# Optimization experiments

Hardware: AMD Instinct MI355X
Metric: run time of the kernel (lower is better)

Reference implementation:

```python
import jax, jax.numpy as jnp
import numpy as np

N_NODES = 100000
N_EDGES = 3200000
N_GRAPHS = 256
FEAT = 128
HIDDEN = 128
N_CLASSES = 10


def setup_inputs() -> dict:
    key = jax.random.key(0)
    ks = jax.random.split(key, 12)
    x = jax.random.normal(ks[0], (N_NODES, FEAT), dtype=jnp.float32)
    edge_index = jax.random.randint(ks[1], (2, N_EDGES), 0, N_NODES, dtype=jnp.int64)
    batch = jnp.sort(jax.random.randint(ks[2], (N_NODES,), 0, N_GRAPHS, dtype=jnp.int64))
    s = 0.05
    return {
        "x": x,
        "edge_index": edge_index,
        "batch": batch,
        "W1": jax.random.normal(ks[3], (FEAT, HIDDEN), dtype=jnp.float32) * s,
        "b1": jnp.zeros((HIDDEN,), dtype=jnp.float32),
        "W2": jax.random.normal(ks[4], (HIDDEN, HIDDEN), dtype=jnp.float32) * s,
        "b2": jnp.zeros((HIDDEN,), dtype=jnp.float32),
        "W3": jax.random.normal(ks[5], (HIDDEN, HIDDEN), dtype=jnp.float32) * s,
        "b3": jnp.zeros((HIDDEN,), dtype=jnp.float32),
        "lin1_w": jax.random.normal(ks[6], (HIDDEN, HIDDEN), dtype=jnp.float32) * s,
        "lin1_b": jnp.zeros((HIDDEN,), dtype=jnp.float32),
        "lin2_w": jax.random.normal(ks[7], (HIDDEN, N_CLASSES), dtype=jnp.float32) * s,
        "lin2_b": jnp.zeros((N_CLASSES,), dtype=jnp.float32),
    }


def _gcn_norm(edge_index, n_nodes):
    # PyG GCNConv default: add self-loops, symmetric normalization.
    src = jnp.concatenate([edge_index[0], jnp.arange(n_nodes, dtype=edge_index.dtype)])
    dst = jnp.concatenate([edge_index[1], jnp.arange(n_nodes, dtype=edge_index.dtype)])
    deg = jax.ops.segment_sum(jnp.ones_like(dst, dtype=jnp.float32), dst, num_segments=n_nodes)
    dis = jnp.where(deg > 0, jax.lax.rsqrt(jnp.maximum(deg, 1.0)), 0.0)
    norm = dis[src] * dis[dst]  # [E + N]
    return src, dst, norm


def _gcn_conv(x, src, dst, norm, W, b, n_nodes):
    h = x @ W                               # [N, H]
    msg = h[src] * norm[:, None]            # gather + scale, [E+N, H]
    out = jax.ops.segment_sum(msg, dst, num_segments=n_nodes)  # scatter-add
    return out + b


def reference(x, edge_index, batch, W1, b1, W2, b2, W3, b3, lin1_w, lin1_b, lin2_w, lin2_b):
    n = x.shape[0]
    src, dst, norm = _gcn_norm(edge_index, n)
    h = jax.nn.relu(_gcn_conv(x, src, dst, norm, W1, b1, n))
    h = jax.nn.relu(_gcn_conv(h, src, dst, norm, W2, b2, n))
    h = jax.nn.relu(_gcn_conv(h, src, dst, norm, W3, b3, n))
    # global mean pool over graphs
    sums = jax.ops.segment_sum(h, batch, num_segments=N_GRAPHS)
    cnts = jax.ops.segment_sum(jnp.ones((n,), dtype=h.dtype), batch, num_segments=N_GRAPHS)
    g = sums / jnp.maximum(cnts, 1.0)[:, None]
    g = jax.nn.relu(g @ lin1_w + lin1_b)
    # dropout p=0.5 is identity at inference
    return g @ lin2_w + lin2_b
```

## Files before the change

### kernel.cpp

```cpp
#include <hip/hip_runtime.h>
#include <hip/hip_fp16.h>

#define FEAT 128
#define CHUNK 8192
#define BSH 7
#define CAP 6144
#define RSTRIDE 784

#define QS  16.0f
#define QSI 0.0625f

typedef _Float16 half8 __attribute__((ext_vector_type(8)));
typedef float floatx4 __attribute__((ext_vector_type(4)));
typedef float floatx2 __attribute__((ext_vector_type(2)));

__device__ __forceinline__ unsigned int enc8x4(float a, float b, float c, float d) {
  unsigned int r = __builtin_amdgcn_cvt_pk_fp8_f32(a, b, 0u, false);
  return __builtin_amdgcn_cvt_pk_fp8_f32(c, d, r, true);
}
__device__ __forceinline__ void acc8(unsigned int w, float* a) {
  floatx2 v0 = __builtin_amdgcn_cvt_pk_f32_fp8(w, false);
  floatx2 v1 = __builtin_amdgcn_cvt_pk_f32_fp8(w, true);
  a[0] += v0.x; a[1] += v0.y; a[2] += v1.x; a[3] += v1.y;
}


__global__ __launch_bounds__(256) void sort_prep_kernel(
    const int* __restrict__ ei, int E, int nchunks, int nbuk,
    int* __restrict__ pairs, int* __restrict__ runs,
    const float* __restrict__ W1, const float* __restrict__ W2,
    const float* __restrict__ W3, _Float16* __restrict__ P1,
    _Float16* __restrict__ P2, _Float16* __restrict__ P3,
    unsigned char* __restrict__ qA, unsigned char* __restrict__ qB, int N) {
  __shared__ int lhist[1024];
  __shared__ int lofs[1024];
  __shared__ int lcur[1024];
  __shared__ int tsum[256];
  __shared__ int stage[CHUNK];
  int t = threadIdx.x;
  if ((int)blockIdx.x >= nchunks) {
    int b = blockIdx.x - nchunks;
    if (b == 24) {
      if (t < 16) ((unsigned long long*)(qA + (size_t)N * FEAT))[t] = 0ull;
      else if (t < 32) ((unsigned long long*)(qB + (size_t)N * FEAT))[t - 16] = 0ull;
      return;
    }
    const float* W = (b < 8) ? W1 : (b < 16) ? W2 : W3;
    _Float16* P = (b < 8) ? P1 : (b < 16) ? P2 : P3;
    int e = (b & 7) * 256 + t;
    int l = e & 63;
    int ks = (e >> 6) & 3;
    int tn = e >> 8;
    int n = tn * 16 + (l & 15);
    int k0 = ks * 32 + (l >> 4) * 8;
    half8 v;
#pragma unroll
    for (int j = 0; j < 8; ++j) v[j] = (_Float16)W[(k0 + j) * 128 + n];
    *(half8*)(P + (size_t)e * 8) = v;
    return;
  }
  int c = blockIdx.x;
  int e0 = c * CHUNK;
  int e1 = e0 + CHUNK; if (e1 > E) e1 = E;
  int cnt = e1 - e0;
#pragma unroll
  for (int u = 0; u < 4; ++u) lhist[t + u * 256] = 0;
  __syncthreads();
  for (int j = e0 + t; j < e1; j += 256) atomicAdd(&lhist[ei[E + j] >> BSH], 1);
  __syncthreads();
  int a0 = lhist[4 * t], a1 = lhist[4 * t + 1];
  int a2 = lhist[4 * t + 2], a3 = lhist[4 * t + 3];
  int s = ((a0 + a1) + (a2 + a3));
  tsum[t] = s;
  __syncthreads();
  for (int o = 1; o < 256; o <<= 1) {
    int x = (t >= o) ? tsum[t - o] : 0;
    __syncthreads();
    tsum[t] += x;
    __syncthreads();
  }
  int base = tsum[t] - s;
  lofs[4 * t] = base;       lcur[4 * t] = base;
  lofs[4 * t + 1] = base + a0;           lcur[4 * t + 1] = base + a0;
  lofs[4 * t + 2] = base + a0 + a1;      lcur[4 * t + 2] = base + a0 + a1;
  lofs[4 * t + 3] = base + a0 + a1 + a2; lcur[4 * t + 3] = base + a0 + a1 + a2;
  __syncthreads();
  for (int k = t; k < nbuk; k += 256) runs[(size_t)c * RSTRIDE + k] = lofs[k];
  if (t == 0) runs[(size_t)c * RSTRIDE + nbuk] = cnt;
  for (int j = e0 + t; j < e1; j += 256) {
    int sv = ei[j];
    int d = ei[E + j];
    int p = atomicAdd(&lcur[d >> BSH], 1);
    stage[p] = sv | ((d & 127) << 24);
  }
  __syncthreads();
  for (int j = t; j < cnt; j += 256) pairs[e0 + j] = stage[j];
}

__global__ __launch_bounds__(256) void bucket_csr_kernel(
    const int* __restrict__ pairs, const int* __restrict__ runs, int nchunks,
    int nbuk, int2* __restrict__ row_se, float* __restrict__ dis,
    int* __restrict__ col, int N) {
  __shared__ int rs[512], rl[512], ro[512];
  __shared__ int cnt2[2048];
  __shared__ int tsum[256];
  __shared__ int stage[CAP];
  int b = blockIdx.x, t = threadIdx.x;
  for (int c = t; c < 512; c += 256) {
    int s0 = 0, len = 0;
    if (c < nchunks) {
      const int* rr = runs + (size_t)c * RSTRIDE;
      s0 = rr[b];
      len = rr[b + 1] - s0;
    }
    rs[c] = s0; rl[c] = len;
  }
#pragma unroll
  for (int u = 0; u < 8; ++u) cnt2[t + u * 256] = 0;
  __syncthreads();
  ro[t] = rl[t]; ro[t + 256] = rl[t + 256];
  __syncthreads();
  for (int o = 1; o < 512; o <<= 1) {
    int v0 = (t >= o) ? ro[t - o] : 0;
    int v1 = (t + 256 >= o) ? ro[t + 256 - o] : 0;
    __syncthreads();
    ro[t] += v0; ro[t + 256] += v1;
    __syncthreads();
  }
  int ce = ro[511];
  int y0 = ro[t] - rl[t];
  int y1 = ro[t + 256] - rl[t + 256];
  __syncthreads();
  ro[t] = y0; ro[t + 256] = y1;
  __syncthreads();
  int colbase = b * CAP;
  bool fits = ce <= CAP;
  if (fits) {
    for (int c = t; c < nchunks; c += 256) {
      int gs = c * CHUNK + rs[c];
      int base = ro[c];
      int len = rl[c];
      for (int j = 0; j < len; ++j) {
        int p = pairs[gs + j];
        stage[base + j] = p;
        int key = (((unsigned)p) >> 24) * 16 + ((p & 0xFFFFFF) >> 13);
        atomicAdd(&cnt2[key], 1);
      }
    }
  } else {
    for (int c = t; c < nchunks; c += 256) {
      int gs = c * CHUNK + rs[c];
      for (int j = 0; j < rl[c]; ++j) {
        int p = pairs[gs + j];
        int key = (((unsigned)p) >> 24) * 16 + ((p & 0xFFFFFF) >> 13);
        atomicAdd(&cnt2[key], 1);
      }
    }
  }
  __syncthreads();
  int av[8];
#pragma unroll
  for (int u = 0; u < 8; ++u) av[u] = cnt2[t * 8 + u];
  int s = 0;
#pragma unroll
  for (int u = 0; u < 8; ++u) s += av[u];
  tsum[t] = s;
  __syncthreads();
  for (int o = 1; o < 256; o <<= 1) {
    int x = (t >= o) ? tsum[t - o] : 0;
    __syncthreads();
    tsum[t] += x;
    __syncthreads();
  }
  int run = tsum[t] - s;
#pragma unroll
  for (int u = 0; u < 8; ++u) { int tmp = av[u]; cnt2[t * 8 + u] = run; run += tmp; }
  __syncthreads();
  if (t < 128) {
    int startv = cnt2[t * 16];
    int endv = (t == 127) ? ce : cnt2[t * 16 + 16];
    int node = b * 128 + t;
    if (node < N) {
      row_se[node] = make_int2(colbase + startv, colbase + endv);
      dis[node] = rsqrtf((float)(endv - startv + 1));
    }
  }
  __syncthreads();
  if (fits) {
    for (int j = t; j < ce; j += 256) {
      int p = stage[j];
      int src = p & 0xFFFFFF;
      int key = (((unsigned)p) >> 24) * 16 + (src >> 13);
      int loc = atomicAdd(&cnt2[key], 1);
      col[colbase + loc] = src << 7;
    }
  } else {
    for (int c = t; c < nchunks; c += 256) {
      int gs = c * CHUNK + rs[c];
      for (int j = 0; j < rl[c]; ++j) {
        int p = pairs[gs + j];
        int src = p & 0xFFFFFF;
        int key = (((unsigned)p) >> 24) * 16 + (src >> 13);
        int loc = atomicAdd(&cnt2[key], 1);
        if (loc < CAP) col[colbase + loc] = src << 7;
      }
    }
  }
}


__global__ __launch_bounds__(256) void mm1_kernel(
    const float* __restrict__ Av, const _Float16* __restrict__ Wpk,
    const float* __restrict__ scale, unsigned char* __restrict__ C, int N) {
  int t = threadIdx.x;
  int wave = t >> 6, lane = t & 63;
  int quad = lane >> 4, nidx = lane & 15;
  int m0 = blockIdx.x * 64 + wave * 16;
  int arow = m0 + nidx;
  bool avalid = arow < N;
  floatx4 acc[8];
#pragma unroll
  for (int tn = 0; tn < 8; ++tn) acc[tn] = (floatx4){0.f, 0.f, 0.f, 0.f};
#pragma unroll
  for (int ks = 0; ks < 4; ++ks) {
    half8 x = {};
    if (avalid) {
      const float* p = Av + (size_t)arow * 128 + ks * 32 + quad * 8;
      float4 f0 = *(const float4*)p;
      float4 f1 = *(const float4*)(p + 4);
      x[0] = (_Float16)f0.x; x[1] = (_Float16)f0.y;
      x[2] = (_Float16)f0.z; x[3] = (_Float16)f0.w;
      x[4] = (_Float16)f1.x; x[5] = (_Float16)f1.y;
      x[6] = (_Float16)f1.z; x[7] = (_Float16)f1.w;
    }
#pragma unroll
    for (int tn = 0; tn < 8; ++tn) {
      half8 wfrag = *(const half8*)(Wpk + ((size_t)((tn * 4 + ks) * 64 + lane)) * 8);
      acc[tn] = __builtin_amdgcn_mfma_f32_16x16x32_f16(wfrag, x, acc[tn], 0, 0, 0);
    }
  }
  if (avalid) {
    float s = scale[arow] * QS;
#pragma unroll
    for (int tn = 0; tn < 8; ++tn) {
      unsigned int r = enc8x4(acc[tn][0] * s, acc[tn][1] * s,
                              acc[tn][2] * s, acc[tn][3] * s);
      *(unsigned int*)(C + (size_t)arow * 128 + tn * 16 + quad * 4) = r;
    }
  }
}

__global__ __launch_bounds__(256) void agg_fuse_kernel(
    const unsigned char* __restrict__ hs_in, const int2* __restrict__ row_se,
    const int* __restrict__ col, const float* __restrict__ dis,
    const float* __restrict__ bias, const _Float16* __restrict__ Wpk,
    unsigned char* __restrict__ hs_out, int N) {
  __shared__ _Float16 Xs[32][136];
  int t = threadIdx.x;
  int wave = t >> 6, lane = t & 63;
  int lin = lane & 7;
  int nl = wave * 8 + (lane >> 3);
  int node = blockIdx.x * 32 + nl;
  bool valid = node < N;
  int lin16 = lin * 16;
  int zoff = N << 7;
  float a[16];
#pragma unroll
  for (int j = 0; j < 16; ++j) a[j] = 0.f;
  int selfoff = (valid ? (node << 7) : zoff) + lin16;
  uint4 s0 = *(const uint4*)(hs_in + (unsigned)selfoff);
  acc8(s0.x, a); acc8(s0.y, a + 4); acc8(s0.z, a + 8); acc8(s0.w, a + 12);
  int2 se = valid ? row_se[node] : make_int2(0, 0);
  int i = se.x, e = se.y;
  while (__any(i < e)) {
    int c[8];
#pragma unroll
    for (int u = 0; u < 8; ++u) {
      int idx = i + u;
      c[u] = (idx < e) ? col[idx] : zoff;
    }
    uint4 r[8];
#pragma unroll
    for (int u = 0; u < 8; ++u)
      r[u] = *(const uint4*)(hs_in + (unsigned)(c[u] + lin16));
#pragma unroll
    for (int u = 0; u < 8; ++u) {
      acc8(r[u].x, a);     acc8(r[u].y, a + 4);
      acc8(r[u].z, a + 8); acc8(r[u].w, a + 12);
    }
    i += 8;
  }
  float d = valid ? dis[node] * QSI : 0.f;
  const float* bp = bias + lin16;
  half8 hx0, hx1;
#pragma unroll
  for (int j = 0; j < 8; ++j) {
    float o0 = valid ? fmaxf(fmaf(d, a[j], bp[j]), 0.f) : 0.f;
    float o1 = valid ? fmaxf(fmaf(d, a[j + 8], bp[j + 8]), 0.f) : 0.f;
    hx0[j] = (_Float16)o0;
    hx1[j] = (_Float16)o1;
  }
  *(half8*)&Xs[nl][lin16] = hx0;
  *(half8*)&Xs[nl][lin16 + 8] = hx1;
  __syncthreads();
  int quad = lane >> 4, nidx = lane & 15;
  int ntile = wave >> 1;
  int f0 = (wave & 1) * 4;
  floatx4 acc[4];
#pragma unroll
  for (int f = 0; f < 4; ++f) acc[f] = (floatx4){0.f, 0.f, 0.f, 0.f};
#pragma unroll
  for (int ks = 0; ks < 4; ++ks) {
    half8 x = *(const half8*)&Xs[ntile * 16 + nidx][ks * 32 + quad * 8];
#pragma unroll
    for (int f = 0; f < 4; ++f) {
      half8 wf = *(const half8*)(Wpk + ((size_t)(((f0 + f) * 4 + ks) * 64 + lane)) * 8);
      acc[f] = __builtin_amdgcn_mfma_f32_16x16x32_f16(wf, x, acc[f], 0, 0, 0);
    }
  }
  int onode = blockIdx.x * 32 + ntile * 16 + nidx;
  if (onode < N) {
    float sc = dis[onode] * QS;
#pragma unroll
    for (int f = 0; f < 4; ++f) {
      unsigned int rq = enc8x4(acc[f][0] * sc, acc[f][1] * sc,
                               acc[f][2] * sc, acc[f][3] * sc);
      *(unsigned int*)(hs_out + (size_t)onode * 128 + (f0 + f) * 16 + quad * 4) = rq;
    }
  }
}

__global__ __launch_bounds__(256) void agg_kernel(
    const unsigned char* __restrict__ hs, const int2* __restrict__ row_se,
    const int* __restrict__ col, const float* __restrict__ dis,
    const float* __restrict__ bias, _Float16* __restrict__ out, int N) {
  int t = threadIdx.x;
  int wave = t >> 6, lane = t & 63;
  int lin = lane & 7;
  int nl = wave * 8 + (lane >> 3);
  int node = blockIdx.x * 32 + nl;
  bool valid = node < N;
  int lin16 = lin * 16;
  int zoff = N << 7;
  float a[16];
#pragma unroll
  for (int j = 0; j < 16; ++j) a[j] = 0.f;
  int selfoff = (valid ? (node << 7) : zoff) + lin16;
  uint4 s0 = *(const uint4*)(hs + (unsigned)selfoff);
  acc8(s0.x, a); acc8(s0.y, a + 4); acc8(s0.z, a + 8); acc8(s0.w, a + 12);
  int2 se = valid ? row_se[node] : make_int2(0, 0);
  int i = se.x, e = se.y;
  while (__any(i < e)) {
    int c[8];
#pragma unroll
    for (int u = 0; u < 8; ++u) {
      int idx = i + u;
      c[u] = (idx < e) ? col[idx] : zoff;
    }
    uint4 r[8];
#pragma unroll
    for (int u = 0; u < 8; ++u)
      r[u] = *(const uint4*)(hs + (unsigned)(c[u] + lin16));
#pragma unroll
    for (int u = 0; u < 8; ++u) {
      acc8(r[u].x, a);     acc8(r[u].y, a + 4);
      acc8(r[u].z, a + 8); acc8(r[u].w, a + 12);
    }
    i += 8;
  }
  if (valid) {
    float d = dis[node] * QSI;
    const float* bp = bias + lin16;
    half8 hx0, hx1;
#pragma unroll
    for (int j = 0; j < 8; ++j) {
      hx0[j] = (_Float16)fmaxf(fmaf(d, a[j], bp[j]), 0.f);
      hx1[j] = (_Float16)fmaxf(fmaf(d, a[j + 8], bp[j + 8]), 0.f);
    }
    *(half8*)(out + (size_t)node * FEAT + lin16) = hx0;
    *(half8*)(out + (size_t)node * FEAT + lin16 + 8) = hx1;
  }
}

__global__ __launch_bounds__(128) void head_kernel(
    const __half* __restrict__ h, const int* __restrict__ batch,
    const float* __restrict__ l1w, const float* __restrict__ l1b,
    const float* __restrict__ l2w, const float* __restrict__ l2b,
    float* __restrict__ out, int N, int C) {
  __shared__ float row[128];
  __shared__ float row2[128];
  int grp = blockIdx.x, t = threadIdx.x;
  int lo = 0, hi = N;
  while (lo < hi) { int m = (lo + hi) >> 1; if (batch[m] < grp) lo = m + 1; else hi = m; }
  int start = lo;
  hi = N;
  while (lo < hi) { int m = (lo + hi) >> 1; if (batch[m] <= grp) lo = m + 1; else hi = m; }
  int end = lo;
  float a0 = 0.f, a1 = 0.f, a2 = 0.f, a3 = 0.f;
  int i = start;
  for (; i + 4 <= end; i += 4) {
    a0 += __half2float(h[(size_t)i * 128 + t]);
    a1 += __half2float(h[(size_t)(i + 1) * 128 + t]);
    a2 += __half2float(h[(size_t)(i + 2) * 128 + t]);
    a3 += __half2float(h[(size_t)(i + 3) * 128 + t]);
  }
  for (; i < end; ++i) a0 += __half2float(h[(size_t)i * 128 + t]);
  float sum = (a0 + a1) + (a2 + a3);
  float cntf = (float)(end - start);
  row[t] = sum / fmaxf(cntf, 1.0f);
  __syncthreads();
  float acc = l1b[t];
#pragma unroll 8
  for (int k = 0; k < 128; ++k) acc = fmaf(row[k], l1w[k * 128 + t], acc);
  row2[t] = fmaxf(acc, 0.f);
  __syncthreads();
  if (t < C) {
    float a = l2b[t];
#pragma unroll 8
    for (int k = 0; k < 128; ++k) a = fmaf(row2[k], l2w[k * C + t], a);
    out[grp * C + t] = a;
  }
}


extern "C" void kernel_launch(void* const* d_in, const int* in_sizes, int n_in,
                              void* d_out, int out_size, void* d_ws, size_t ws_size,
                              hipStream_t stream) {
  const float* x   = (const float*)d_in[0];
  const int*   ei  = (const int*)d_in[1];
  const int*   bat = (const int*)d_in[2];
  const float* W1  = (const float*)d_in[3];
  const float* b1  = (const float*)d_in[4];
  const float* W2  = (const float*)d_in[5];
  const float* b2  = (const float*)d_in[6];
  const float* W3  = (const float*)d_in[7];
  const float* b3  = (const float*)d_in[8];
  const float* l1w = (const float*)d_in[9];
  const float* l1b = (const float*)d_in[10];
  const float* l2w = (const float*)d_in[11];
  const float* l2b = (const float*)d_in[12];

  int N = in_sizes[2];
  int E = in_sizes[1] / 2;
  int C = in_sizes[12];
  int G = out_size / C;
  float* outp = (float*)d_out;

  char* wp = (char*)d_ws;
  auto alloc = [&](size_t bytes) -> void* {
    void* p = (void*)wp;
    wp += (bytes + 255) & ~(size_t)255;
    return p;
  };
  int nbuk    = (N + 127) / 128;
  int nchunks = (E + CHUNK - 1) / CHUNK;

  float*    dis    = (float*)alloc((size_t)N * 4);
  int2*     row_se = (int2*)alloc((size_t)N * 8);
  int*      col    = (int*)alloc((size_t)nbuk * CAP * 4);
  int*      pairs  = (int*)alloc((size_t)nchunks * CHUNK * 4);
  int*      runs   = (int*)alloc((size_t)nchunks * RSTRIDE * 4);
  _Float16* Wpk1   = (_Float16*)alloc(16384 * 2);
  _Float16* Wpk2   = (_Float16*)alloc(16384 * 2);
  _Float16* Wpk3   = (_Float16*)alloc(16384 * 2);
  unsigned char* qA = (unsigned char*)alloc((size_t)(N + 1) * FEAT);
  unsigned char* qB = (unsigned char*)alloc((size_t)(N + 1) * FEAT);
  _Float16* hout  = (_Float16*)alloc((size_t)N * FEAT * 2);

  sort_prep_kernel<<<nchunks + 25, 256, 0, stream>>>(
      ei, E, nchunks, nbuk, pairs, runs, W1, W2, W3, Wpk1, Wpk2, Wpk3,
      qA, qB, N);
  bucket_csr_kernel<<<nbuk, 256, 0, stream>>>(pairs, runs, nchunks, nbuk,
                                              row_se, dis, col, N);

  int mmB = (N + 63) / 64;
  int gB  = (N + 31) / 32;

  mm1_kernel<<<mmB, 256, 0, stream>>>(x, Wpk1, dis, qA, N);
  agg_fuse_kernel<<<gB, 256, 0, stream>>>(qA, row_se, col, dis, b1,
                                          Wpk2, qB, N);
  agg_fuse_kernel<<<gB, 256, 0, stream>>>(qB, row_se, col, dis, b2,
                                          Wpk3, qA, N);
  agg_kernel<<<gB, 256, 0, stream>>>(qA, row_se, col, dis, b3, hout, N);
  head_kernel<<<G, 128, 0, stream>>>((const __half*)hout, bat, l1w, l1b,
                                     l2w, l2b, outp, N, C);
}
```

Before: 460.8 us.

## Use persistent fixed-grid aggregation blocks with segmented neighbor loops

The aggregation kernels now launch a fixed grid of 1024 blocks, and each block loops over several 32-node tiles instead of one block per tile. Each node's neighbor list is split into 8 segments, and each segment is processed in unrolled groups of 4 gathers instead of groups of 8. The goal is to cut block launch overhead and lower per-thread register pressure for better occupancy. In exchange, the segmentation adds loop overhead and extra wave-level any-checks, fewer gathers are in flight per iteration, and the fused kernel needs an extra barrier per tile.

```diff
diff --git a/kernel.cpp b/kernel.cpp
--- a/kernel.cpp
+++ b/kernel.cpp
@@ -6,6 +6,7 @@
 #define BSH 7
 #define CAP 6144
 #define RSTRIDE 784
+#define GBLK 1024
 
 #define QS  16.0f
 #define QSI 0.0625f
@@ -254,131 +255,147 @@
     const unsigned char* __restrict__ hs_in, const int2* __restrict__ row_se,
     const int* __restrict__ col, const float* __restrict__ dis,
     const float* __restrict__ bias, const _Float16* __restrict__ Wpk,
-    unsigned char* __restrict__ hs_out, int N) {
+    unsigned char* __restrict__ hs_out, int N, int ntiles) {
   __shared__ _Float16 Xs[32][136];
   int t = threadIdx.x;
   int wave = t >> 6, lane = t & 63;
-  int lin = lane & 7;
-  int nl = wave * 8 + (lane >> 3);
-  int node = blockIdx.x * 32 + nl;
-  bool valid = node < N;
+  int g = t >> 3;
+  int lin = t & 7;
   int lin16 = lin * 16;
   int zoff = N << 7;
-  float a[16];
-#pragma unroll
-  for (int j = 0; j < 16; ++j) a[j] = 0.f;
-  int selfoff = (valid ? (node << 7) : zoff) + lin16;
-  uint4 s0 = *(const uint4*)(hs_in + (unsigned)selfoff);
-  acc8(s0.x, a); acc8(s0.y, a + 4); acc8(s0.z, a + 8); acc8(s0.w, a + 12);
-  int2 se = valid ? row_se[node] : make_int2(0, 0);
-  int i = se.x, e = se.y;
-  while (__any(i < e)) {
-    int c[8];
-#pragma unroll
-    for (int u = 0; u < 8; ++u) {
-      int idx = i + u;
-      c[u] = (idx < e) ? col[idx] : zoff;
-    }
-    uint4 r[8];
-#pragma unroll
-    for (int u = 0; u < 8; ++u)
-      r[u] = *(const uint4*)(hs_in + (unsigned)(c[u] + lin16));
-#pragma unroll
-    for (int u = 0; u < 8; ++u) {
-      acc8(r[u].x, a);     acc8(r[u].y, a + 4);
-      acc8(r[u].z, a + 8); acc8(r[u].w, a + 12);
-    }
-    i += 8;
-  }
-  float d = valid ? dis[node] * QSI : 0.f;
-  const float* bp = bias + lin16;
-  half8 hx0, hx1;
-#pragma unroll
-  for (int j = 0; j < 8; ++j) {
-    float o0 = valid ? fmaxf(fmaf(d, a[j], bp[j]), 0.f) : 0.f;
-    float o1 = valid ? fmaxf(fmaf(d, a[j + 8], bp[j + 8]), 0.f) : 0.f;
-    hx0[j] = (_Float16)o0;
-    hx1[j] = (_Float16)o1;
-  }
-  *(half8*)&Xs[nl][lin16] = hx0;
-  *(half8*)&Xs[nl][lin16 + 8] = hx1;
-  __syncthreads();
   int quad = lane >> 4, nidx = lane & 15;
-  int ntile = wave >> 1;
-  int f0 = (wave & 1) * 4;
-  floatx4 acc[4];
-#pragma unroll
-  for (int f = 0; f < 4; ++f) acc[f] = (floatx4){0.f, 0.f, 0.f, 0.f};
-#pragma unroll
-  for (int ks = 0; ks < 4; ++ks) {
-    half8 x = *(const half8*)&Xs[ntile * 16 + nidx][ks * 32 + quad * 8];
-#pragma unroll
-    for (int f = 0; f < 4; ++f) {
-      half8 wf = *(const half8*)(Wpk + ((size_t)(((f0 + f) * 4 + ks) * 64 + lane)) * 8);
-      acc[f] = __builtin_amdgcn_mfma_f32_16x16x32_f16(wf, x, acc[f], 0, 0, 0);
-    }
-  }
-  int onode = blockIdx.x * 32 + ntile * 16 + nidx;
-  if (onode < N) {
-    float sc = dis[onode] * QS;
-#pragma unroll
-    for (int f = 0; f < 4; ++f) {
-      unsigned int rq = enc8x4(acc[f][0] * sc, acc[f][1] * sc,
-                               acc[f][2] * sc, acc[f][3] * sc);
-      *(unsigned int*)(hs_out + (size_t)onode * 128 + (f0 + f) * 16 + quad * 4) = rq;
-    }
+  int base0 = blockIdx.x * ntiles * 32;
+#pragma unroll 1
+  for (int s = 0; s < ntiles; ++s) {
+    int nb = base0 + s * 32;
+    int node = nb + g;
+    bool valid = node < N;
+    float a[16];
+#pragma unroll
+    for (int j = 0; j < 16; ++j) a[j] = 0.f;
+    int selfoff = (valid ? (node << 7) : zoff) + lin16;
+    uint4 sv = *(const uint4*)(hs_in + (unsigned)selfoff);
+    acc8(sv.x, a); acc8(sv.y, a + 4); acc8(sv.z, a + 8); acc8(sv.w, a + 12);
+    int2 se = valid ? row_se[node] : make_int2(0, 0);
+    int ib = se.x, deg = se.y - se.x;
+#pragma unroll 1
+    for (int k = 0; k < 8; ++k) {
+      int j  = ib + ((k * deg) >> 3);
+      int je = ib + (((k + 1) * deg) >> 3);
+      while (__any(j < je)) {
+        int c[4];
+#pragma unroll
+        for (int u = 0; u < 4; ++u)
+          c[u] = (j + u < je) ? col[j + u] : zoff;
+        uint4 r[4];
+#pragma unroll
+        for (int u = 0; u < 4; ++u)
+          r[u] = *(const uint4*)(hs_in + (unsigned)(c[u] + lin16));
+#pragma unroll
+        for (int u = 0; u < 4; ++u) {
+          acc8(r[u].x, a);     acc8(r[u].y, a + 4);
+          acc8(r[u].z, a + 8); acc8(r[u].w, a + 12);
+        }
+        j += 4;
+      }
+    }
+    float dd = valid ? dis[node] * QSI : 0.f;
+    const float* bp = bias + lin16;
+    half8 hx0, hx1;
+#pragma unroll
+    for (int j = 0; j < 8; ++j) {
+      float o0 = valid ? fmaxf(fmaf(dd, a[j], bp[j]), 0.f) : 0.f;
+      float o1 = valid ? fmaxf(fmaf(dd, a[j + 8], bp[j + 8]), 0.f) : 0.f;
+      hx0[j] = (_Float16)o0;
+      hx1[j] = (_Float16)o1;
+    }
+    *(half8*)&Xs[g][lin16] = hx0;
+    *(half8*)&Xs[g][lin16 + 8] = hx1;
+    __syncthreads();
+    int ntile = wave >> 1;
+    int f0 = (wave & 1) * 4;
+    floatx4 acc[4];
+#pragma unroll
+    for (int f = 0; f < 4; ++f) acc[f] = (floatx4){0.f, 0.f, 0.f, 0.f};
+#pragma unroll
+    for (int ks = 0; ks < 4; ++ks) {
+      half8 x = *(const half8*)&Xs[ntile * 16 + nidx][ks * 32 + quad * 8];
+#pragma unroll
+      for (int f = 0; f < 4; ++f) {
+        half8 wf = *(const half8*)(Wpk + ((size_t)(((f0 + f) * 4 + ks) * 64 + lane)) * 8);
+        acc[f] = __builtin_amdgcn_mfma_f32_16x16x32_f16(wf, x, acc[f], 0, 0, 0);
+      }
+    }
+    int onode = nb + ntile * 16 + nidx;
+    if (onode < N) {
+      float sc = dis[onode] * QS;
+#pragma unroll
+      for (int f = 0; f < 4; ++f) {
+        unsigned int rq = enc8x4(acc[f][0] * sc, acc[f][1] * sc,
+                                 acc[f][2] * sc, acc[f][3] * sc);
+        *(unsigned int*)(hs_out + (size_t)onode * 128 + (f0 + f) * 16 + quad * 4) = rq;
+      }
+    }
+    __syncthreads();
   }
 }
 
 __global__ __launch_bounds__(256) void agg_kernel(
     const unsigned char* __restrict__ hs, const int2* __restrict__ row_se,
     const int* __restrict__ col, const float* __restrict__ dis,
-    const float* __restrict__ bias, _Float16* __restrict__ out, int N) {
+    const float* __restrict__ bias, _Float16* __restrict__ out, int N,
+    int ntiles) {
   int t = threadIdx.x;
-  int wave = t >> 6, lane = t & 63;
-  int lin = lane & 7;
-  int nl = wave * 8 + (lane >> 3);
-  int node = blockIdx.x * 32 + nl;
-  bool valid = node < N;
+  int g = t >> 3;
+  int lin = t & 7;
   int lin16 = lin * 16;
   int zoff = N << 7;
-  float a[16];
-#pragma unroll
-  for (int j = 0; j < 16; ++j) a[j] = 0.f;
-  int selfoff = (valid ? (node << 7) : zoff) + lin16;
-  uint4 s0 = *(const uint4*)(hs + (unsigned)selfoff);
-  acc8(s0.x, a); acc8(s0.y, a + 4); acc8(s0.z, a + 8); acc8(s0.w, a + 12);
-  int2 se = valid ? row_se[node] : make_int2(0, 0);
-  int i = se.x, e = se.y;
-  while (__any(i < e)) {
-    int c[8];
-#pragma unroll
-    for (int u = 0; u < 8; ++u) {
-      int idx = i + u;
-      c[u] = (idx < e) ? col[idx] : zoff;
-    }
-    uint4 r[8];
-#pragma unroll
-    for (int u = 0; u < 8; ++u)
-      r[u] = *(const uint4*)(hs + (unsigned)(c[u] + lin16));
-#pragma unroll
-    for (int u = 0; u < 8; ++u) {
-      acc8(r[u].x, a);     acc8(r[u].y, a + 4);
-      acc8(r[u].z, a + 8); acc8(r[u].w, a + 12);
-    }
-    i += 8;
-  }
-  if (valid) {
-    float d = dis[node] * QSI;
-    const float* bp = bias + lin16;
-    half8 hx0, hx1;
-#pragma unroll
-    for (int j = 0; j < 8; ++j) {
-      hx0[j] = (_Float16)fmaxf(fmaf(d, a[j], bp[j]), 0.f);
-      hx1[j] = (_Float16)fmaxf(fmaf(d, a[j + 8], bp[j + 8]), 0.f);
-    }
-    *(half8*)(out + (size_t)node * FEAT + lin16) = hx0;
-    *(half8*)(out + (size_t)node * FEAT + lin16 + 8) = hx1;
+  int base0 = blockIdx.x * ntiles * 32;
+#pragma unroll 1
+  for (int s = 0; s < ntiles; ++s) {
+    int node = base0 + s * 32 + g;
+    bool valid = node < N;
+    float a[16];
+#pragma unroll
+    for (int j = 0; j < 16; ++j) a[j] = 0.f;
+    int selfoff = (valid ? (node << 7) : zoff) + lin16;
+    uint4 sv = *(const uint4*)(hs + (unsigned)selfoff);
+    acc8(sv.x, a); acc8(sv.y, a + 4); acc8(sv.z, a + 8); acc8(sv.w, a + 12);
+    int2 se = valid ? row_se[node] : make_int2(0, 0);
+    int ib = se.x, deg = se.y - se.x;
+#pragma unroll 1
+    for (int k = 0; k < 8; ++k) {
+      int j  = ib + ((k * deg) >> 3);
+      int je = ib + (((k + 1) * deg) >> 3);
+      while (__any(j < je)) {
+        int c[4];
+#pragma unroll
+        for (int u = 0; u < 4; ++u)
+          c[u] = (j + u < je) ? col[j + u] : zoff;
+        uint4 r[4];
+#pragma unroll
+        for (int u = 0; u < 4; ++u)
+          r[u] = *(const uint4*)(hs + (unsigned)(c[u] + lin16));
+#pragma unroll
+        for (int u = 0; u < 4; ++u) {
+          acc8(r[u].x, a);     acc8(r[u].y, a + 4);
+          acc8(r[u].z, a + 8); acc8(r[u].w, a + 12);
+        }
+        j += 4;
+      }
+    }
+    if (valid) {
+      float dd = dis[node] * QSI;
+      const float* bp = bias + lin16;
+      half8 hx0, hx1;
+#pragma unroll
+      for (int j = 0; j < 8; ++j) {
+        hx0[j] = (_Float16)fmaxf(fmaf(dd, a[j], bp[j]), 0.f);
+        hx1[j] = (_Float16)fmaxf(fmaf(dd, a[j + 8], bp[j + 8]), 0.f);
+      }
+      *(half8*)(out + (size_t)node * FEAT + lin16) = hx0;
+      *(half8*)(out + (size_t)node * FEAT + lin16 + 8) = hx1;
+    }
   }
 }
 
@@ -474,14 +491,15 @@
                                               row_se, dis, col, N);
 
   int mmB = (N + 63) / 64;
-  int gB  = (N + 31) / 32;
+  int ntiles = (N + GBLK * 32 - 1) / (GBLK * 32);
 
   mm1_kernel<<<mmB, 256, 0, stream>>>(x, Wpk1, dis, qA, N);
-  agg_fuse_kernel<<<gB, 256, 0, stream>>>(qA, row_se, col, dis, b1,
-                                          Wpk2, qB, N);
-  agg_fuse_kernel<<<gB, 256, 0, stream>>>(qB, row_se, col, dis, b2,
-                                          Wpk3, qA, N);
-  agg_kernel<<<gB, 256, 0, stream>>>(qA, row_se, col, dis, b3, hout, N);
+  agg_fuse_kernel<<<GBLK, 256, 0, stream>>>(qA, row_se, col, dis, b1,
+                                            Wpk2, qB, N, ntiles);
+  agg_fuse_kernel<<<GBLK, 256, 0, stream>>>(qB, row_se, col, dis, b2,
+                                            Wpk3, qA, N, ntiles);
+  agg_kernel<<<GBLK, 256, 0, stream>>>(qA, row_se, col, dis, b3, hout, N,
+                                       ntiles);
   head_kernel<<<G, 128, 0, stream>>>((const __half*)hout, bat, l1w, l1b,
                                      l2w, l2b, outp, N, C);
 }
```

After: 587.1 us. +27.4%, slower.
